# Kernel optimization log

Hardware: AMD Instinct MI355X
Metric: run time of the kernel (lower is better)

## Reference

```python
import jax, jax.numpy as jnp
import numpy as np

DIM = 512
HEAD_DIM = 32
NUM_HEADS = DIM // HEAD_DIM
SCALE = HEAD_DIM ** -0.5
SPARSE_WINDOW = 64
LN_EPS = 1e-5


def setup_inputs() -> dict:
    key = jax.random.key(0)
    ks = jax.random.split(key, 7)
    B, S = 2, 2048
    x = jax.random.normal(ks[0], (B, S, DIM), dtype=jnp.float32)
    # parameters (Linear weights stored as [in, out] for x @ W)
    W_qkv = jax.random.normal(ks[1], (DIM, 2 * DIM), dtype=jnp.float32) * (DIM ** -0.5)
    b_qkv = jnp.zeros((2 * DIM,), dtype=jnp.float32)
    W_out = jax.random.normal(ks[2], (DIM, DIM), dtype=jnp.float32) * (DIM ** -0.5)
    b_out = jnp.zeros((DIM,), dtype=jnp.float32)
    ln_gamma = jnp.ones((DIM,), dtype=jnp.float32)
    ln_beta = jnp.zeros((DIM,), dtype=jnp.float32)
    return {"x": x, "W_qkv": W_qkv, "b_qkv": b_qkv, "W_out": W_out,
            "b_out": b_out, "ln_gamma": ln_gamma, "ln_beta": ln_beta}


def _attn(x, W_qkv, b_qkv, W_out, b_out, ln_gamma, ln_beta):
    B, S, _ = x.shape
    qkv = x @ W_qkv + b_qkv                        # [B,S,2*DIM]
    qk, v = qkv[..., :DIM], qkv[..., DIM:]
    q = jax.nn.silu(qk) * SCALE                    # shared-projection nonlinear Q
    k = jnp.tanh(qk)                               # shared-projection nonlinear K
    q = q.reshape(B, S, NUM_HEADS, HEAD_DIM)
    k = k.reshape(B, S, NUM_HEADS, HEAD_DIM)
    v = v.reshape(B, S, NUM_HEADS, HEAD_DIM)
    scores = jnp.einsum('bihd,bjhd->bhij', q, k)   # [B,H,S,S]
    # sparse window: MULTIPLICATIVE zeroing outside |i-j|<=w (faithful to source)
    i = jnp.arange(S)
    band = (jnp.abs(i[:, None] - i[None, :]) <= SPARSE_WINDOW).astype(scores.dtype)
    scores = scores * band                         # zeros still enter softmax as exp(0)
    probs = jax.nn.softmax(scores, axis=-1)
    out = jnp.einsum('bhij,bjhd->bihd', probs, v).reshape(B, S, DIM)
    out = out @ W_out + b_out
    y = x + out                                    # residual (dropout is eval no-op)
    mu = jnp.mean(y, axis=-1, keepdims=True)
    var = jnp.var(y, axis=-1, keepdims=True)
    return (y - mu) * jax.lax.rsqrt(var + LN_EPS) * ln_gamma + ln_beta


def reference(x, W_qkv, b_qkv, W_out, b_out, ln_gamma, ln_beta):
    return _attn(x, W_qkv, b_qkv, W_out, b_out, ln_gamma, ln_beta)
```

## Files before the change

### kernel.cpp

```cpp
#include <hip/hip_runtime.h>
#include <cstdint>
#include <cstddef>

#define DIMX 512
#define HDIM 32
#define NHEADS 16
#define SEQ 2048
#define BATCH 2
#define MTOT (BATCH*SEQ)
#define WIN 64
#define QSCALE 0.17677669529663687f

typedef __bf16 bf16x8 __attribute__((ext_vector_type(8)));
typedef float f32x4 __attribute__((ext_vector_type(4)));

__device__ __forceinline__ unsigned short f2bf(float f){
  unsigned u = __builtin_bit_cast(unsigned, f);
  u += 0x7FFFu + ((u >> 16) & 1u);
  return (unsigned short)(u >> 16);
}
__device__ __forceinline__ float bf2f(unsigned short s){
  return __builtin_bit_cast(float, ((unsigned)s) << 16);
}
__device__ __forceinline__ unsigned pk(float a, float b){
  return (unsigned)f2bf(a) | ((unsigned)f2bf(b) << 16);
}

__device__ __forceinline__ void gl_lds16(const void* g, void* l){
  __builtin_amdgcn_global_load_lds(
      (const __attribute__((address_space(1))) unsigned*)g,
      (__attribute__((address_space(3))) unsigned*)(unsigned)(unsigned long long)l,
      16, 0, 0);
}

template<int N> __device__ __forceinline__ void vmwait(){
  if      constexpr (N == 12) asm volatile("s_waitcnt vmcnt(12)" ::: "memory");
  else if constexpr (N ==  8) asm volatile("s_waitcnt vmcnt(8)"  ::: "memory");
  else if constexpr (N ==  6) asm volatile("s_waitcnt vmcnt(6)"  ::: "memory");
  else if constexpr (N ==  4) asm volatile("s_waitcnt vmcnt(4)"  ::: "memory");
  else                        asm volatile("s_waitcnt vmcnt(0)"  ::: "memory");
}

__global__ void k_prep(const float* __restrict__ x, unsigned short* __restrict__ xb,
                       const float* __restrict__ Wq, unsigned short* __restrict__ Wqt,
                       const float* __restrict__ Wo, unsigned short* __restrict__ Wot){
  int bx = blockIdx.x;
  if (bx < 1024){
    int i = bx * 256 + threadIdx.x;
    const float4* p = (const float4*)x + (size_t)i * 2;
    float4 a = p[0], b = p[1];
    uint4 o;
    o.x = pk(a.x, a.y); o.y = pk(a.z, a.w);
    o.z = pk(b.x, b.y); o.w = pk(b.z, b.w);
    ((uint4*)xb)[i] = o;
    return;
  }
  __shared__ float tile[32][33];
  int i = bx - 1024;
  int bxx = i % 48, byy = i / 48;
  const float* W; unsigned short* Wt; int N, n0;
  if (bxx < 32){ W = Wq; Wt = Wqt; N = 1024; n0 = bxx * 32; }
  else         { W = Wo; Wt = Wot; N = 512;  n0 = (bxx - 32) * 32; }
  int k0 = byy * 32;
  int tx = threadIdx.x & 31, ty = threadIdx.x >> 5;
  #pragma unroll
  for (int r = 0; r < 32; r += 8)
    tile[ty + r][tx] = W[(size_t)(k0 + ty + r) * N + n0 + tx];
  __syncthreads();
  #pragma unroll
  for (int r = 0; r < 32; r += 8)
    Wt[(size_t)(n0 + ty + r) * 512 + k0 + tx] = f2bf(tile[tx][ty + r]);
}

template<int MODE, int BM, int NBM, int NBN>
__launch_bounds__(256)
__global__ void k_gemm(const unsigned short* __restrict__ A,
                       const unsigned short* __restrict__ Bt,
                       const float* __restrict__ bias,
                       unsigned short* __restrict__ qb,
                       unsigned short* __restrict__ kb,
                       unsigned short* __restrict__ vt,
                       float* __restrict__ vsum_p,
                       const unsigned short* __restrict__ xb,
                       unsigned short* __restrict__ yb)
{
  const int K = 512;
  constexpr int NWG = NBM * NBN;
  constexpr int MF  = BM / 32;
  constexpr int LPS = MF + 2;
  __shared__ __align__(16) unsigned short ldsA[3][BM * 64];
  __shared__ __align__(16) unsigned short ldsB[3][64 * 64];
  int tid = threadIdx.x;
  int wid = tid >> 6, lane = tid & 63;
  int wm = wid >> 1, wn = wid & 1;
  int lane15 = lane & 15, laneh = lane >> 4;

  int g = blockIdx.x;
  int gwi = (g & 7) * (NWG / 8) + (g >> 3);
  int bm = gwi / NBN, bn = gwi % NBN;

  f32x4 acc[MF][2] = {};

  int srow_off = lane >> 3;
  int spos     = lane & 7;

  auto STAGE = [&](int buf, int kt){
    int k0 = kt * 64;
    #pragma unroll
    for (int c = 0; c < MF; ++c){
      int cidx = wid * MF + c;
      int r = cidx * 8 + srow_off;
      int ch = spos ^ (r & 7);
      gl_lds16(A + (size_t)(bm * BM + r) * K + k0 + ch * 8, &ldsA[buf][cidx * 512]);
    }
    #pragma unroll
    for (int c = 0; c < 2; ++c){
      int cidx = wid * 2 + c;
      int r = cidx * 8 + srow_off;
      int ch = spos ^ (r & 7);
      gl_lds16(Bt + (size_t)(bn * 64 + r) * K + k0 + ch * 8, &ldsB[buf][cidx * 512]);
    }
  };

  auto COMPUTE = [&](int buf){
    #pragma unroll
    for (int kh = 0; kh < 2; ++kh){
      int chunk = kh * 4 + laneh;
      bf16x8 af[MF], bfv[2];
      #pragma unroll
      for (int mi = 0; mi < MF; ++mi){
        int row = wm * (BM / 2) + mi * 16 + lane15;
        af[mi] = *(const bf16x8*)&ldsA[buf][row * 64 + (chunk ^ (row & 7)) * 8];
      }
      #pragma unroll
      for (int ni = 0; ni < 2; ++ni){
        int row = wn * 32 + ni * 16 + lane15;
        bfv[ni] = *(const bf16x8*)&ldsB[buf][row * 64 + (chunk ^ (row & 7)) * 8];
      }
      #pragma unroll
      for (int mi = 0; mi < MF; ++mi)
        #pragma unroll
        for (int ni = 0; ni < 2; ++ni)
          acc[mi][ni] = __builtin_amdgcn_mfma_f32_16x16x32_bf16(af[mi], bfv[ni], acc[mi][ni], 0, 0, 0);
    }
  };

  STAGE(0, 0);
  STAGE(1, 1);
  #pragma unroll
  for (int kt = 0; kt < 8; ++kt){
    if (kt < 6) STAGE((kt + 2) % 3, kt + 2);
    if (kt < 6)       vmwait<2 * LPS>();
    else if (kt == 6) vmwait<LPS>();
    else              vmwait<0>();
    __builtin_amdgcn_s_barrier();
    __builtin_amdgcn_sched_barrier(0);
    COMPUTE(kt % 3);
    __builtin_amdgcn_s_barrier();
    __builtin_amdgcn_sched_barrier(0);
  }

  if (MODE == 0 && bn >= 8){
    unsigned short (*tp)[136] = (unsigned short (*)[136])&ldsA[0][0];
    #pragma unroll
    for (int mi = 0; mi < MF; ++mi)
      #pragma unroll
      for (int ni = 0; ni < 2; ++ni)
        #pragma unroll
        for (int r = 0; r < 4; ++r){
          int ml = wm * (BM / 2) + mi * 16 + laneh * 4 + r;
          int nl = wn * 32 + ni * 16 + lane15;
          tp[nl][ml] = f2bf(acc[mi][ni][r] + bias[bn * 64 + nl]);
        }
    __syncthreads();
    int nl = tid >> 2, q = tid & 3;
    int h = (bn - 8) * 2 + (nl >> 5), d = nl & 31;
    int b = bm >> 4, sc = bm & 15;
    int bh = b * 16 + h;
    uint4 v4[4];
    float ssum = 0.f;
    #pragma unroll
    for (int p = 0; p < 4; ++p){
      v4[p] = *(const uint4*)&tp[nl][q * 32 + p * 8];
      const unsigned* w = (const unsigned*)&v4[p];
      #pragma unroll
      for (int j = 0; j < 4; ++j){
        ssum += bf2f((unsigned short)(w[j] & 0xffff)) + bf2f((unsigned short)(w[j] >> 16));
      }
    }
    ssum += __shfl_xor(ssum, 1); ssum += __shfl_xor(ssum, 2);
    size_t vtoff = (size_t)(bh * HDIM + d) * SEQ + sc * 128 + q * 32;
    #pragma unroll
    for (int p = 0; p < 4; ++p) *(uint4*)(vt + vtoff + p * 8) = v4[p];
    if (q == 0) vsum_p[(sc * 32 + bh) * HDIM + d] = ssum;
  } else {
    #pragma unroll
    for (int mi = 0; mi < MF; ++mi){
      #pragma unroll
      for (int ni = 0; ni < 2; ++ni){
        #pragma unroll
        for (int r = 0; r < 4; ++r){
          int m = bm * BM + wm * (BM / 2) + mi * 16 + laneh * 4 + r;
          int n = bn * 64 + wn * 32 + ni * 16 + lane15;
          float val = acc[mi][ni][r] + bias[n];
          if (MODE == 0){
            float s = val / (1.0f + __expf(-val)) * QSCALE;
            float t = 1.0f - 2.0f / (1.0f + __expf(2.0f * val));
            qb[(size_t)m * DIMX + n] = f2bf(s);
            kb[(size_t)m * DIMX + n] = f2bf(t);
          } else {
            size_t idx = (size_t)m * DIMX + n;
            yb[idx] = f2bf(val + bf2f(xb[idx]));
          }
        }
      }
    }
  }
}

__launch_bounds__(256)
__global__ void k_attn(const unsigned short* __restrict__ qb,
                       const unsigned short* __restrict__ kb,
                       const unsigned short* __restrict__ vt,
                       const float* __restrict__ vsum_p,
                       unsigned short* __restrict__ ao)
{
  __shared__ unsigned short p_lds[4][16][40];
  int tid = threadIdx.x, wid = tid >> 6, lane = tid & 63;
  int lane15 = lane & 15, laneh = lane >> 4;
  int bh = blockIdx.y, b = bh >> 4, h = bh & 15;
  int s0 = blockIdx.x * 64 + wid * 16;

  bf16x8 qf = *(const bf16x8*)(qb + (size_t)(b * SEQ + s0 + lane15) * DIMX + h * HDIM + laneh * 8);
  float vs0 = 0.f, vs1 = 0.f;
  #pragma unroll
  for (int c = 0; c < 16; ++c){
    vs0 += vsum_p[(c * 32 + bh) * HDIM + lane15];
    vs1 += vsum_p[(c * 32 + bh) * HDIM + 16 + lane15];
  }

  f32x4 accv[2] = {};
  float dsum[4] = {0.f, 0.f, 0.f, 0.f};

  for (int jt = 0; jt < 9; ++jt){
    int j0 = s0 - 64 + jt * 16;
    int jc = min(max(j0 + lane15, 0), SEQ - 1);
    bf16x8 kf = *(const bf16x8*)(kb + (size_t)(b * SEQ + jc) * DIMX + h * HDIM + laneh * 8);
    f32x4 z = {0.f, 0.f, 0.f, 0.f};
    f32x4 sv = __builtin_amdgcn_mfma_f32_16x16x32_bf16(qf, kf, z, 0, 0, 0);
    #pragma unroll
    for (int r = 0; r < 4; ++r){
      int i = s0 + laneh * 4 + r;
      int j = j0 + lane15;
      int dj = i - j;
      bool inb = (dj <= WIN) && (dj >= -WIN) && (j >= 0) && (j < SEQ);
      float w = inb ? (__expf(sv[r]) - 1.0f) : 0.0f;
      dsum[r] += w;
      p_lds[wid][laneh * 4 + r][(jt & 1) * 16 + lane15] = f2bf(w);
    }
    if (jt & 1){
      int jc0 = j0 - 16;
      bf16x8 pa = *(const bf16x8*)&p_lds[wid][lane15][laneh * 8];
      int jv = min(max(jc0 + laneh * 8, 0), SEQ - 8);
      bf16x8 v0 = *(const bf16x8*)(vt + (size_t)(bh * HDIM + lane15) * SEQ + jv);
      bf16x8 v1 = *(const bf16x8*)(vt + (size_t)(bh * HDIM + 16 + lane15) * SEQ + jv);
      accv[0] = __builtin_amdgcn_mfma_f32_16x16x32_bf16(pa, v0, accv[0], 0, 0, 0);
      accv[1] = __builtin_amdgcn_mfma_f32_16x16x32_bf16(pa, v1, accv[1], 0, 0, 0);
    }
  }
  {
    #pragma unroll
    for (int r = 0; r < 4; ++r)
      p_lds[wid][laneh * 4 + r][16 + lane15] = 0;
    int jc0 = s0 + 64;
    bf16x8 pa = *(const bf16x8*)&p_lds[wid][lane15][laneh * 8];
    int jv = min(max(jc0 + laneh * 8, 0), SEQ - 8);
    bf16x8 v0 = *(const bf16x8*)(vt + (size_t)(bh * HDIM + lane15) * SEQ + jv);
    bf16x8 v1 = *(const bf16x8*)(vt + (size_t)(bh * HDIM + 16 + lane15) * SEQ + jv);
    accv[0] = __builtin_amdgcn_mfma_f32_16x16x32_bf16(pa, v0, accv[0], 0, 0, 0);
    accv[1] = __builtin_amdgcn_mfma_f32_16x16x32_bf16(pa, v1, accv[1], 0, 0, 0);
  }

  #pragma unroll
  for (int r = 0; r < 4; ++r){
    float v = dsum[r];
    v += __shfl_xor(v, 1); v += __shfl_xor(v, 2);
    v += __shfl_xor(v, 4); v += __shfl_xor(v, 8);
    dsum[r] = v;
  }
  #pragma unroll
  for (int r = 0; r < 4; ++r){
    int i = s0 + laneh * 4 + r;
    float dn = (float)SEQ + dsum[r];
    float o0 = (accv[0][r] + vs0) / dn;
    float o1 = (accv[1][r] + vs1) / dn;
    size_t base = (size_t)(b * SEQ + i) * DIMX + h * HDIM;
    ao[base + lane15]      = f2bf(o0);
    ao[base + 16 + lane15] = f2bf(o1);
  }
}

__global__ void k_ln(const unsigned short* __restrict__ yb, const float* __restrict__ gamma,
                     const float* __restrict__ beta, float* __restrict__ out){
  int wid = threadIdx.x >> 6, lane = threadIdx.x & 63;
  int row = blockIdx.x * 4 + wid;
  uint4 u = *(const uint4*)(yb + (size_t)row * DIMX + lane * 8);
  const unsigned* w = (const unsigned*)&u;
  float v[8];
  #pragma unroll
  for (int j = 0; j < 4; ++j){
    v[2*j]   = bf2f((unsigned short)(w[j] & 0xffff));
    v[2*j+1] = bf2f((unsigned short)(w[j] >> 16));
  }
  float s = 0.f, ss = 0.f;
  #pragma unroll
  for (int j = 0; j < 8; ++j){ s += v[j]; ss += v[j] * v[j]; }
  #pragma unroll
  for (int m = 1; m < 64; m <<= 1){ s += __shfl_xor(s, m); ss += __shfl_xor(ss, m); }
  float mu = s * (1.f / DIMX);
  float var = ss * (1.f / DIMX) - mu * mu;
  float inv = rsqrtf(var + 1e-5f);
  float4 g0 = *(const float4*)(gamma + lane * 8);
  float4 g1 = *(const float4*)(gamma + lane * 8 + 4);
  float4 b0 = *(const float4*)(beta + lane * 8);
  float4 b1 = *(const float4*)(beta + lane * 8 + 4);
  float4 o0, o1;
  o0.x = (v[0] - mu) * inv * g0.x + b0.x; o0.y = (v[1] - mu) * inv * g0.y + b0.y;
  o0.z = (v[2] - mu) * inv * g0.z + b0.z; o0.w = (v[3] - mu) * inv * g0.w + b0.w;
  o1.x = (v[4] - mu) * inv * g1.x + b1.x; o1.y = (v[5] - mu) * inv * g1.y + b1.y;
  o1.z = (v[6] - mu) * inv * g1.z + b1.z; o1.w = (v[7] - mu) * inv * g1.w + b1.w;
  float* op = out + (size_t)row * DIMX + lane * 8;
  *(float4*)op = o0; *(float4*)(op + 4) = o1;
}

extern "C" void kernel_launch(void* const* d_in, const int* in_sizes, int n_in,
                              void* d_out, int out_size, void* d_ws, size_t ws_size,
                              hipStream_t stream){
  const float* x      = (const float*)d_in[0];
  const float* W_qkv  = (const float*)d_in[1];
  const float* b_qkv  = (const float*)d_in[2];
  const float* W_out  = (const float*)d_in[3];
  const float* b_out  = (const float*)d_in[4];
  const float* gamma  = (const float*)d_in[5];
  const float* beta   = (const float*)d_in[6];
  float* out = (float*)d_out;

  char* ws = (char*)d_ws;
  size_t off = 0;
  auto alloc = [&](size_t bytes){ void* p = ws + off; off += (bytes + 255) & ~(size_t)255; return p; };
  unsigned short* xb  = (unsigned short*)alloc((size_t)MTOT * DIMX * 2);
  unsigned short* wqt = (unsigned short*)alloc((size_t)1024 * 512 * 2);
  unsigned short* wot = (unsigned short*)alloc((size_t)512 * 512 * 2);
  unsigned short* qb  = (unsigned short*)alloc((size_t)MTOT * DIMX * 2);
  unsigned short* kb  = (unsigned short*)alloc((size_t)MTOT * DIMX * 2);
  unsigned short* vt  = (unsigned short*)alloc((size_t)32 * HDIM * SEQ * 2);
  float*          vsm = (float*)alloc((size_t)16 * 32 * HDIM * 4);
  unsigned short* ao  = (unsigned short*)alloc((size_t)MTOT * DIMX * 2);
  unsigned short* yb  = (unsigned short*)alloc((size_t)MTOT * DIMX * 2);

  k_prep<<<1792, 256, 0, stream>>>(x, xb, W_qkv, wqt, W_out, wot);
  k_gemm<0, 128, 32, 16><<<512, 256, 0, stream>>>(xb, wqt, b_qkv, qb, kb, vt, vsm, nullptr, nullptr);
  k_attn<<<dim3(32, 32), 256, 0, stream>>>(qb, kb, vt, vsm, ao);
  k_gemm<1, 64, 64, 8><<<512, 256, 0, stream>>>(ao, wot, b_out, nullptr, nullptr, nullptr, nullptr, xb, yb);
  k_ln  <<<MTOT / 4, 256, 0, stream>>>(yb, gamma, beta, out);
}
```

Baseline: 46.06 us.

## Use 128x128 QKV GEMM tiles and head-major Q/K layout for attention

Splits the templated GEMM into two kernels. The QKV projection now runs 256 workgroups of 512 threads on 128x128 tiles with a shared LDS buffer. Q and K are written in a head-major [b,h,s,d] layout so the attention kernel reads each head's rows contiguously instead of striding by the model dimension. The goals are more operand reuse per tile and better-coalesced loads in attention. In exchange there are fewer workgroups, more LDS per block, and scattered 2-byte epilogue stores.

```diff
diff --git a/kernel.cpp b/kernel.cpp
--- a/kernel.cpp
+++ b/kernel.cpp
@@ -34,9 +34,8 @@
 }
 
 template<int N> __device__ __forceinline__ void vmwait(){
-  if      constexpr (N == 12) asm volatile("s_waitcnt vmcnt(12)" ::: "memory");
+  if      constexpr (N == 16) asm volatile("s_waitcnt vmcnt(16)" ::: "memory");
   else if constexpr (N ==  8) asm volatile("s_waitcnt vmcnt(8)"  ::: "memory");
-  else if constexpr (N ==  6) asm volatile("s_waitcnt vmcnt(6)"  ::: "memory");
   else if constexpr (N ==  4) asm volatile("s_waitcnt vmcnt(4)"  ::: "memory");
   else                        asm volatile("s_waitcnt vmcnt(0)"  ::: "memory");
 }
@@ -72,34 +71,28 @@
     Wt[(size_t)(n0 + ty + r) * 512 + k0 + tx] = f2bf(tile[tx][ty + r]);
 }
 
-template<int MODE, int BM, int NBM, int NBN>
-__launch_bounds__(256)
-__global__ void k_gemm(const unsigned short* __restrict__ A,
-                       const unsigned short* __restrict__ Bt,
-                       const float* __restrict__ bias,
-                       unsigned short* __restrict__ qb,
-                       unsigned short* __restrict__ kb,
-                       unsigned short* __restrict__ vt,
-                       float* __restrict__ vsum_p,
-                       const unsigned short* __restrict__ xb,
-                       unsigned short* __restrict__ yb)
+__launch_bounds__(512)
+__global__ void k_gemm0(const unsigned short* __restrict__ A,
+                        const unsigned short* __restrict__ Bt,
+                        const float* __restrict__ bias,
+                        unsigned short* __restrict__ qb,
+                        unsigned short* __restrict__ kb,
+                        unsigned short* __restrict__ vt,
+                        float* __restrict__ vsum_p)
 {
   const int K = 512;
-  constexpr int NWG = NBM * NBN;
-  constexpr int MF  = BM / 32;
-  constexpr int LPS = MF + 2;
-  __shared__ __align__(16) unsigned short ldsA[3][BM * 64];
-  __shared__ __align__(16) unsigned short ldsB[3][64 * 64];
+  constexpr int NWG = 256;
+  __shared__ __align__(16) unsigned short lds[3][256 * 64];
   int tid = threadIdx.x;
   int wid = tid >> 6, lane = tid & 63;
-  int wm = wid >> 1, wn = wid & 1;
+  int wm = wid >> 2, wn = wid & 3;
   int lane15 = lane & 15, laneh = lane >> 4;
 
   int g = blockIdx.x;
   int gwi = (g & 7) * (NWG / 8) + (g >> 3);
-  int bm = gwi / NBN, bn = gwi % NBN;
-
-  f32x4 acc[MF][2] = {};
+  int bm = gwi / 8, bn = gwi % 8;
+
+  f32x4 acc[4][2] = {};
 
   int srow_off = lane >> 3;
   int spos     = lane & 7;
@@ -107,18 +100,18 @@
   auto STAGE = [&](int buf, int kt){
     int k0 = kt * 64;
     #pragma unroll
-    for (int c = 0; c < MF; ++c){
-      int cidx = wid * MF + c;
-      int r = cidx * 8 + srow_off;
-      int ch = spos ^ (r & 7);
-      gl_lds16(A + (size_t)(bm * BM + r) * K + k0 + ch * 8, &ldsA[buf][cidx * 512]);
-    }
-    #pragma unroll
-    for (int c = 0; c < 2; ++c){
-      int cidx = wid * 2 + c;
-      int r = cidx * 8 + srow_off;
-      int ch = spos ^ (r & 7);
-      gl_lds16(Bt + (size_t)(bn * 64 + r) * K + k0 + ch * 8, &ldsB[buf][cidx * 512]);
+    for (int c = 0; c < 4; ++c){
+      int g2 = wid * 4 + c;
+      if (g2 < 16){
+        int r = g2 * 8 + srow_off;
+        int ch = spos ^ (r & 7);
+        gl_lds16(A + (size_t)(bm * 128 + r) * K + k0 + ch * 8, &lds[buf][g2 * 512]);
+      } else {
+        int gb = g2 - 16;
+        int r = gb * 8 + srow_off;
+        int ch = spos ^ (r & 7);
+        gl_lds16(Bt + (size_t)(bn * 128 + r) * K + k0 + ch * 8, &lds[buf][8192 + gb * 512]);
+      }
     }
   };
 
@@ -126,19 +119,19 @@
     #pragma unroll
     for (int kh = 0; kh < 2; ++kh){
       int chunk = kh * 4 + laneh;
-      bf16x8 af[MF], bfv[2];
-      #pragma unroll
-      for (int mi = 0; mi < MF; ++mi){
-        int row = wm * (BM / 2) + mi * 16 + lane15;
-        af[mi] = *(const bf16x8*)&ldsA[buf][row * 64 + (chunk ^ (row & 7)) * 8];
+      bf16x8 af[4], bfv[2];
+      #pragma unroll
+      for (int mi = 0; mi < 4; ++mi){
+        int row = wm * 64 + mi * 16 + lane15;
+        af[mi] = *(const bf16x8*)&lds[buf][row * 64 + (chunk ^ (row & 7)) * 8];
       }
       #pragma unroll
       for (int ni = 0; ni < 2; ++ni){
         int row = wn * 32 + ni * 16 + lane15;
-        bfv[ni] = *(const bf16x8*)&ldsB[buf][row * 64 + (chunk ^ (row & 7)) * 8];
-      }
-      #pragma unroll
-      for (int mi = 0; mi < MF; ++mi)
+        bfv[ni] = *(const bf16x8*)&lds[buf][8192 + row * 64 + (chunk ^ (row & 7)) * 8];
+      }
+      #pragma unroll
+      for (int mi = 0; mi < 4; ++mi)
         #pragma unroll
         for (int ni = 0; ni < 2; ++ni)
           acc[mi][ni] = __builtin_amdgcn_mfma_f32_16x16x32_bf16(af[mi], bfv[ni], acc[mi][ni], 0, 0, 0);
@@ -150,8 +143,8 @@
   #pragma unroll
   for (int kt = 0; kt < 8; ++kt){
     if (kt < 6) STAGE((kt + 2) % 3, kt + 2);
-    if (kt < 6)       vmwait<2 * LPS>();
-    else if (kt == 6) vmwait<LPS>();
+    if (kt < 6)       vmwait<8>();
+    else if (kt == 6) vmwait<4>();
     else              vmwait<0>();
     __builtin_amdgcn_s_barrier();
     __builtin_amdgcn_sched_barrier(0);
@@ -160,21 +153,21 @@
     __builtin_amdgcn_sched_barrier(0);
   }
 
-  if (MODE == 0 && bn >= 8){
-    unsigned short (*tp)[136] = (unsigned short (*)[136])&ldsA[0][0];
-    #pragma unroll
-    for (int mi = 0; mi < MF; ++mi)
+  if (bn >= 4){
+    unsigned short (*tp)[136] = (unsigned short (*)[136])&lds[0][0];
+    #pragma unroll
+    for (int mi = 0; mi < 4; ++mi)
       #pragma unroll
       for (int ni = 0; ni < 2; ++ni)
         #pragma unroll
         for (int r = 0; r < 4; ++r){
-          int ml = wm * (BM / 2) + mi * 16 + laneh * 4 + r;
+          int ml = wm * 64 + mi * 16 + laneh * 4 + r;
           int nl = wn * 32 + ni * 16 + lane15;
-          tp[nl][ml] = f2bf(acc[mi][ni][r] + bias[bn * 64 + nl]);
+          tp[nl][ml] = f2bf(acc[mi][ni][r] + bias[bn * 128 + nl]);
         }
     __syncthreads();
     int nl = tid >> 2, q = tid & 3;
-    int h = (bn - 8) * 2 + (nl >> 5), d = nl & 31;
+    int h = (bn - 4) * 4 + (nl >> 5), d = nl & 31;
     int b = bm >> 4, sc = bm & 15;
     int bh = b * 16 + h;
     uint4 v4[4];
@@ -184,9 +177,8 @@
       v4[p] = *(const uint4*)&tp[nl][q * 32 + p * 8];
       const unsigned* w = (const unsigned*)&v4[p];
       #pragma unroll
-      for (int j = 0; j < 4; ++j){
+      for (int j = 0; j < 4; ++j)
         ssum += bf2f((unsigned short)(w[j] & 0xffff)) + bf2f((unsigned short)(w[j] >> 16));
-      }
     }
     ssum += __shfl_xor(ssum, 1); ssum += __shfl_xor(ssum, 2);
     size_t vtoff = (size_t)(bh * HDIM + d) * SEQ + sc * 128 + q * 32;
@@ -195,24 +187,119 @@
     if (q == 0) vsum_p[(sc * 32 + bh) * HDIM + d] = ssum;
   } else {
     #pragma unroll
-    for (int mi = 0; mi < MF; ++mi){
+    for (int mi = 0; mi < 4; ++mi){
       #pragma unroll
       for (int ni = 0; ni < 2; ++ni){
         #pragma unroll
         for (int r = 0; r < 4; ++r){
-          int m = bm * BM + wm * (BM / 2) + mi * 16 + laneh * 4 + r;
-          int n = bn * 64 + wn * 32 + ni * 16 + lane15;
+          int m = bm * 128 + wm * 64 + mi * 16 + laneh * 4 + r;
+          int n = bn * 128 + wn * 32 + ni * 16 + lane15;
           float val = acc[mi][ni][r] + bias[n];
-          if (MODE == 0){
-            float s = val / (1.0f + __expf(-val)) * QSCALE;
-            float t = 1.0f - 2.0f / (1.0f + __expf(2.0f * val));
-            qb[(size_t)m * DIMX + n] = f2bf(s);
-            kb[(size_t)m * DIMX + n] = f2bf(t);
-          } else {
-            size_t idx = (size_t)m * DIMX + n;
-            yb[idx] = f2bf(val + bf2f(xb[idx]));
-          }
+          int b = m >> 11, s = m & 2047;
+          int h = n >> 5, d = n & 31;
+          size_t idx = ((size_t)(b * 16 + h) * SEQ + s) * HDIM + d;
+          float sv = val / (1.0f + __expf(-val)) * QSCALE;
+          float tv = 1.0f - 2.0f / (1.0f + __expf(2.0f * val));
+          qb[idx] = f2bf(sv);
+          kb[idx] = f2bf(tv);
         }
+      }
+    }
+  }
+}
+
+__launch_bounds__(256)
+__global__ void k_gemm1(const unsigned short* __restrict__ A,
+                        const unsigned short* __restrict__ Bt,
+                        const float* __restrict__ bias,
+                        const unsigned short* __restrict__ xb,
+                        unsigned short* __restrict__ yb)
+{
+  const int K = 512;
+  constexpr int NWG = 512;
+  constexpr int LPS = 4;
+  __shared__ __align__(16) unsigned short lds[3][128 * 64];
+  int tid = threadIdx.x;
+  int wid = tid >> 6, lane = tid & 63;
+  int wm = wid >> 1, wn = wid & 1;
+  int lane15 = lane & 15, laneh = lane >> 4;
+
+  int g = blockIdx.x;
+  int gwi = (g & 7) * (NWG / 8) + (g >> 3);
+  int bm = gwi / 8, bn = gwi % 8;
+
+  f32x4 acc[2][2] = {};
+
+  int srow_off = lane >> 3;
+  int spos     = lane & 7;
+
+  auto STAGE = [&](int buf, int kt){
+    int k0 = kt * 64;
+    #pragma unroll
+    for (int c = 0; c < 2; ++c){
+      int cidx = wid * 2 + c;
+      int r = cidx * 8 + srow_off;
+      int ch = spos ^ (r & 7);
+      gl_lds16(A + (size_t)(bm * 64 + r) * K + k0 + ch * 8, &lds[buf][cidx * 512]);
+    }
+    #pragma unroll
+    for (int c = 0; c < 2; ++c){
+      int cidx = wid * 2 + c;
+      int r = cidx * 8 + srow_off;
+      int ch = spos ^ (r & 7);
+      gl_lds16(Bt + (size_t)(bn * 64 + r) * K + k0 + ch * 8, &lds[buf][4096 + cidx * 512]);
+    }
+  };
+
+  auto COMPUTE = [&](int buf){
+    #pragma unroll
+    for (int kh = 0; kh < 2; ++kh){
+      int chunk = kh * 4 + laneh;
+      bf16x8 af[2], bfv[2];
+      #pragma unroll
+      for (int mi = 0; mi < 2; ++mi){
+        int row = wm * 32 + mi * 16 + lane15;
+        af[mi] = *(const bf16x8*)&lds[buf][row * 64 + (chunk ^ (row & 7)) * 8];
+      }
+      #pragma unroll
+      for (int ni = 0; ni < 2; ++ni){
+        int row = wn * 32 + ni * 16 + lane15;
+        bfv[ni] = *(const bf16x8*)&lds[buf][4096 + row * 64 + (chunk ^ (row & 7)) * 8];
+      }
+      #pragma unroll
+      for (int mi = 0; mi < 2; ++mi)
+        #pragma unroll
+        for (int ni = 0; ni < 2; ++ni)
+          acc[mi][ni] = __builtin_amdgcn_mfma_f32_16x16x32_bf16(af[mi], bfv[ni], acc[mi][ni], 0, 0, 0);
+    }
+  };
+
+  STAGE(0, 0);
+  STAGE(1, 1);
+  #pragma unroll
+  for (int kt = 0; kt < 8; ++kt){
+    if (kt < 6) STAGE((kt + 2) % 3, kt + 2);
+    if (kt < 6)       vmwait<8>();
+    else if (kt == 6) vmwait<4>();
+    else              vmwait<0>();
+    __builtin_amdgcn_s_barrier();
+    __builtin_amdgcn_sched_barrier(0);
+    COMPUTE(kt % 3);
+    __builtin_amdgcn_s_barrier();
+    __builtin_amdgcn_sched_barrier(0);
+  }
+
+  #pragma unroll
+  for (int mi = 0; mi < 2; ++mi){
+    #pragma unroll
+    for (int ni = 0; ni < 2; ++ni){
+      #pragma unroll
+      for (int r = 0; r < 4; ++r){
+        int m = bm * 64 + wm * 32 + mi * 16 + laneh * 4 + r;
+        int n = bn * 64 + wn * 32 + ni * 16 + lane15;
+        float val = acc[mi][ni][r] + bias[n];
+        size_t idx = (size_t)m * DIMX + n;
+        yb[idx] = f2bf(val + bf2f(xb[idx]));
       }
     }
   }
@@ -231,7 +318,7 @@
   int bh = blockIdx.y, b = bh >> 4, h = bh & 15;
   int s0 = blockIdx.x * 64 + wid * 16;
 
-  bf16x8 qf = *(const bf16x8*)(qb + (size_t)(b * SEQ + s0 + lane15) * DIMX + h * HDIM + laneh * 8);
+  bf16x8 qf = *(const bf16x8*)(qb + ((size_t)bh * SEQ + s0 + lane15) * HDIM + laneh * 8);
   float vs0 = 0.f, vs1 = 0.f;
   #pragma unroll
   for (int c = 0; c < 16; ++c){
@@ -245,7 +332,7 @@
   for (int jt = 0; jt < 9; ++jt){
     int j0 = s0 - 64 + jt * 16;
     int jc = min(max(j0 + lane15, 0), SEQ - 1);
-    bf16x8 kf = *(const bf16x8*)(kb + (size_t)(b * SEQ + jc) * DIMX + h * HDIM + laneh * 8);
+    bf16x8 kf = *(const bf16x8*)(kb + ((size_t)bh * SEQ + jc) * HDIM + laneh * 8);
     f32x4 z = {0.f, 0.f, 0.f, 0.f};
     f32x4 sv = __builtin_amdgcn_mfma_f32_16x16x32_bf16(qf, kf, z, 0, 0, 0);
     #pragma unroll
@@ -358,9 +445,9 @@
   unsigned short* ao  = (unsigned short*)alloc((size_t)MTOT * DIMX * 2);
   unsigned short* yb  = (unsigned short*)alloc((size_t)MTOT * DIMX * 2);
 
-  k_prep<<<1792, 256, 0, stream>>>(x, xb, W_qkv, wqt, W_out, wot);
-  k_gemm<0, 128, 32, 16><<<512, 256, 0, stream>>>(xb, wqt, b_qkv, qb, kb, vt, vsm, nullptr, nullptr);
-  k_attn<<<dim3(32, 32), 256, 0, stream>>>(qb, kb, vt, vsm, ao);
-  k_gemm<1, 64, 64, 8><<<512, 256, 0, stream>>>(ao, wot, b_out, nullptr, nullptr, nullptr, nullptr, xb, yb);
-  k_ln  <<<MTOT / 4, 256, 0, stream>>>(yb, gamma, beta, out);
-}
+  k_prep <<<1792, 256, 0, stream>>>(x, xb, W_qkv, wqt, W_out, wot);
+  k_gemm0<<<256, 512, 0, stream>>>(xb, wqt, b_qkv, qb, kb, vt, vsm);
+  k_attn <<<dim3(32, 32), 256, 0, stream>>>(qb, kb, vt, vsm, ao);
+  k_gemm1<<<512, 256, 0, stream>>>(ao, wot, b_out, xb, yb);
+  k_ln   <<<MTOT / 4, 256, 0, stream>>>(yb, gamma, beta, out);
+}
```

Result: faster. 43.88 us (-4.7%).
